# Performance work log

Measured on AMD Instinct MI355X. Metric: run time of the kernel, lower is better.

## Reference

```python
import jax, jax.numpy as jnp
import numpy as np

N = 20000      # nodes
C = 64         # in_channels
E = 640000     # edges (avg degree 32)
B = 8          # graphs in batch
STEPS = 16     # 2**4 diffusion steps per cascade
FENG = np.array([4, 8, 9, 12, 13, 14])  # feng_filters()


def make_wavelet():
    # Fixed 4x17 wavelet constructor: Psi_j = P^{2^{j-1}} - P^{2^j}
    W = jnp.zeros((4, 17), dtype=jnp.float32)
    W = W.at[0, 1].set(-1.0).at[0, 2].set(1.0)
    W = W.at[1, 2].set(-1.0).at[1, 4].set(1.0)
    W = W.at[2, 4].set(-1.0).at[2, 8].set(1.0)
    W = W.at[3, 8].set(-1.0).at[3, 16].set(1.0)
    return W


def setup_inputs() -> dict:
    key = jax.random.key(0)
    k1, k2, k3 = jax.random.split(key, 3)
    x = jax.random.normal(k1, (N, C), dtype=jnp.float32)
    edge_index = jax.random.randint(k2, (2, E), 0, N, dtype=jnp.int32)
    batch = jnp.sort(jax.random.randint(k3, (N,), 0, B, dtype=jnp.int32))
    wavelet_constructor = make_wavelet()
    return {"x": x, "edge_index": edge_index, "batch": batch,
            "wavelet_constructor": wavelet_constructor}


def _gcn_norm(edge_index, n, dtype):
    # Add self loops; norm = d^-1/2[row] * d^-1/2[col] (gcn_norm, weight 1)
    row, col = edge_index
    loop = jnp.arange(n, dtype=row.dtype)
    row = jnp.concatenate([row, loop])
    col = jnp.concatenate([col, loop])
    deg = jax.ops.segment_sum(jnp.ones_like(row, dtype=dtype), col, num_segments=n)
    dinv = jnp.where(deg > 0, jax.lax.rsqrt(deg), 0.0)
    return row, col, dinv[row] * dinv[col]


def _cascade(h0, row, col, norm, n):
    # 16 lazy-random-walk diffusion steps: h <- 0.5*(h + A_hat h); keep all levels.
    nb = norm.reshape((-1,) + (1,) * (h0.ndim - 1))
    def step(h, _):
        msg = jax.ops.segment_sum(h[row] * nb, col, num_segments=n)
        h = 0.5 * (h + msg)
        return h, h
    _, ys = jax.lax.scan(step, h0, None, length=STEPS)
    return jnp.concatenate([h0[None], ys], axis=0)  # [17, ...]


def reference(x, edge_index, batch, wavelet_constructor):
    n = x.shape[0]
    row, col, norm = _gcn_norm(edge_index, n, x.dtype)

    # First-order scattering
    S0 = x[:, :, None]                                       # [N, C, 1]
    lev1 = _cascade(S0, row, col, norm, n)                   # [17, N, C, 1]
    sub1 = jnp.einsum('wl,lnck->wnck', wavelet_constructor, lev1)[..., 0]  # [4, N, C]
    S1 = jnp.abs(jnp.transpose(sub1, (1, 2, 0)))             # [N, C, 4]

    # Second-order scattering
    lev2 = _cascade(S1, row, col, norm, n)                   # [17, N, C, 4]
    sub2 = jnp.einsum('wl,lncb->wncb', wavelet_constructor, lev2)          # [4, N, C, 4]
    S2_swapped = jnp.abs(jnp.transpose(sub2, (1, 0, 3, 2))).reshape(n, 16, -1)  # [N, 16, C]
    S2 = S2_swapped[:, FENG]                                 # [N, 6, C]

    feats = jnp.concatenate(
        [jnp.transpose(jnp.concatenate([S0, S1], axis=2), (0, 2, 1)), S2], axis=1)  # [N, 11, C]

    # Statistical-moments aggregation per graph
    d = feats.reshape(n, -1)                                 # [N, 11*C]
    cnt = jnp.maximum(jax.ops.segment_sum(jnp.ones((n,), d.dtype), batch,
                                          num_segments=B), 1.0)[:, None]
    mean = jax.ops.segment_sum(d, batch, num_segments=B) / cnt
    dev = d - mean[batch]
    var = jax.ops.segment_sum(dev ** 2, batch, num_segments=B) / cnt
    m3 = jax.ops.segment_sum(dev ** 3, batch, num_segments=B) / cnt
    m4 = jax.ops.segment_sum(dev ** 4, batch, num_segments=B) / cnt
    safe = var > 0
    vsafe = jnp.where(safe, var, 1.0)
    skew = jnp.where(safe, m3 / vsafe ** 1.5, 0.0)   # NaN (zero-var) -> 0
    kurt = jnp.where(safe, m4 / vsafe ** 2, -3.0)    # NaN (zero-var) -> -3
    out = jnp.concatenate([mean, var, skew, kurt], axis=1)   # [B, 4*11*C]
    return out, wavelet_constructor
```

## Files before the change

### kernel.cpp

```cpp
#include <hip/hip_runtime.h>
#include <hip/hip_fp16.h>

#define NB 8
#define CAP 128
#define NFEAT 704
#define MSLICE 8
#define PSLICE (MSLICE * 4)


__global__ void count_edges(const int* __restrict__ ei, int E, int* __restrict__ cnt) {
    int e = blockIdx.x * blockDim.x + threadIdx.x;
    if (e < E) atomicAdd(&cnt[ei[E + e]], 1);
}

__global__ void compute_dinv(const int* __restrict__ cnt, float* __restrict__ dinv, int n) {
    int v = blockIdx.x * blockDim.x + threadIdx.x;
    if (v < n) dinv[v] = rsqrtf((float)(cnt[v] + 1));
}

__global__ void fill_edges(const int* __restrict__ ei, int E, const float* __restrict__ dinv,
                           int* __restrict__ cursor, unsigned int* __restrict__ pairs) {
    int e = blockIdx.x * blockDim.x + threadIdx.x;
    if (e < E) {
        int r = ei[e], c = ei[E + e];
        int pos = atomicAdd(&cursor[c], 1);
        if (pos < CAP) {
            float w = dinv[r] * dinv[c];
            __half hw = __float2half_rn(w);
            unsigned short hb = *reinterpret_cast<unsigned short*>(&hw);
            pairs[(size_t)c * CAP + pos] = (unsigned int)(r & 0xFFFF) | ((unsigned int)hb << 16);
        }
    }
}

__global__ void pad_edges(const int* __restrict__ cnt, unsigned int* __restrict__ pairs, int n) {
    int v = blockIdx.x * blockDim.x + threadIdx.x;
    if (v >= n) return;
    int c = min(cnt[v], CAP);
    int c4 = (c + 3) & ~3;
    for (int j = c; j < c4; ++j) pairs[(size_t)v * CAP + j] = 0u;
}

__global__ void batch_bounds(const int* __restrict__ batch, int n, int* __restrict__ boff) {
    int i = blockIdx.x * blockDim.x + threadIdx.x;
    if (i >= n) return;
    int b = batch[i];
    int pb = (i == 0) ? -1 : batch[i - 1];
    for (int k = pb + 1; k <= b; ++k) boff[k] = i;
    if (i == n - 1) {
        for (int k = b + 1; k <= NB; ++k) boff[k] = n;
    }
}

__global__ void convert_f16(const float* __restrict__ x, unsigned short* __restrict__ xh, int n) {
    int i = blockIdx.x * blockDim.x + threadIdx.x;
    if (i < n) {
        __half h = __float2half_rn(x[i]);
        xh[i] = *reinterpret_cast<unsigned short*>(&h);
    }
}


__device__ __forceinline__ float h2f16(unsigned short h) {
    __half hh = *reinterpret_cast<__half*>(&h);
    return __half2float(hh);
}

__device__ __forceinline__ void fma_h4(float w, uint2 m, float* a) {
    float2 f0 = __half22float2(*reinterpret_cast<__half2*>(&m.x));
    float2 f1 = __half22float2(*reinterpret_cast<__half2*>(&m.y));
    a[0] += w * f0.x; a[1] += w * f0.y; a[2] += w * f1.x; a[3] += w * f1.y;
}

template <int NU>
__global__ __launch_bounds__(256) void cascade_k(
    const float* __restrict__ selfp, int sstride, long usz,
    const unsigned short* __restrict__ mirp, long musz,
    float* __restrict__ state_out, unsigned short* __restrict__ mir_out,
    const unsigned int* __restrict__ pairs, const int* __restrict__ cnt,
    const float* __restrict__ dinv, int n,
    int s,
    float* __restrict__ prevb,
    float* __restrict__ S1, unsigned short* __restrict__ S1h,
    float* __restrict__ S2)
{
    int lane = threadIdx.x & 63, widx = threadIdx.x >> 6;
    int node = blockIdx.x * 4 + widx;
    if (node >= n) return;
    node = __builtin_amdgcn_readfirstlane(node);

    int deg = min(cnt[node], CAP);
    int deg4 = (deg + 3) & ~3;
    float dv = dinv[node];
    float selfw = 1.f + dv * dv;

    int sub = lane >> 4;
    int cg  = lane & 15;

    const unsigned int* pb = pairs + (size_t)node * CAP;

    float a[NU][4];
#pragma unroll
    for (int u = 0; u < NU; ++u)
#pragma unroll
        for (int k = 0; k < 4; ++k) a[u][k] = 0.f;

    int j = 0;
    for (; j + 8 <= deg4; j += 8) {
        uint4 qA = *reinterpret_cast<const uint4*>(pb + j);
        uint4 qB = *reinterpret_cast<const uint4*>(pb + j + 4);
        unsigned int eA = sub < 2 ? (sub == 0 ? qA.x : qA.y) : (sub == 2 ? qA.z : qA.w);
        unsigned int eB = sub < 2 ? (sub == 0 ? qB.x : qB.y) : (sub == 2 ? qB.z : qB.w);
        int   sA = (int)(eA & 0xFFFFu);
        float wA = h2f16((unsigned short)(eA >> 16));
        int   sB = (int)(eB & 0xFFFFu);
        float wB = h2f16((unsigned short)(eB >> 16));
        uint2 gA[NU], gB[NU];
#pragma unroll
        for (int u = 0; u < NU; ++u)
            gA[u] = *reinterpret_cast<const uint2*>(mirp + (size_t)u * musz + (size_t)sA * 64 + cg * 4);
#pragma unroll
        for (int u = 0; u < NU; ++u)
            gB[u] = *reinterpret_cast<const uint2*>(mirp + (size_t)u * musz + (size_t)sB * 64 + cg * 4);
#pragma unroll
        for (int u = 0; u < NU; ++u) {
            fma_h4(wA, gA[u], a[u]);
            fma_h4(wB, gB[u], a[u]);
        }
    }
    if (j < deg4) {
        uint4 qA = *reinterpret_cast<const uint4*>(pb + j);
        unsigned int eA = sub < 2 ? (sub == 0 ? qA.x : qA.y) : (sub == 2 ? qA.z : qA.w);
        int   sA = (int)(eA & 0xFFFFu);
        float wA = h2f16((unsigned short)(eA >> 16));
        uint2 gA[NU];
#pragma unroll
        for (int u = 0; u < NU; ++u)
            gA[u] = *reinterpret_cast<const uint2*>(mirp + (size_t)u * musz + (size_t)sA * 64 + cg * 4);
#pragma unroll
        for (int u = 0; u < NU; ++u) fma_h4(wA, gA[u], a[u]);
    }

#pragma unroll
    for (int m = 16; m <= 32; m <<= 1) {
#pragma unroll
        for (int u = 0; u < NU; ++u) {
#pragma unroll
            for (int k = 0; k < 4; ++k) a[u][k] += __shfl_xor(a[u][k], m, 64);
        }
    }

    if (lane < 16) {
#pragma unroll
        for (int u = 0; u < NU; ++u) {
            const float* srow = selfp + (size_t)u * usz + (size_t)node * sstride + cg * 4;
            float4 hv = *reinterpret_cast<const float4*>(srow);
            float4 v;
            v.x = 0.5f * (selfw * hv.x + a[u][0]);
            v.y = 0.5f * (selfw * hv.y + a[u][1]);
            v.z = 0.5f * (selfw * hv.z + a[u][2]);
            v.w = 0.5f * (selfw * hv.w + a[u][3]);
            size_t oidx = (size_t)u * n * 64 + (size_t)node * 64 + cg * 4;
            *reinterpret_cast<float4*>(state_out + oidx) = v;
            __half2 p01 = __float22half2_rn(make_float2(v.x, v.y));
            __half2 p23 = __float22half2_rn(make_float2(v.z, v.w));
            uint2 mo;
            mo.x = *reinterpret_cast<unsigned int*>(&p01);
            mo.y = *reinterpret_cast<unsigned int*>(&p23);
            *reinterpret_cast<uint2*>(mir_out + oidx) = mo;

            int snap = (NU == 1) ? 1 : (2 << u);
            float* prow = prevb + oidx;
            if (s == snap) {
                *reinterpret_cast<float4*>(prow) = v;
            } else if (s > snap && (s == 2 || s == 4 || s == 8 || s == 16)) {
                float4 pv = *reinterpret_cast<const float4*>(prow);
                *reinterpret_cast<float4*>(prow) = v;
                float4 d;
                d.x = fabsf(v.x - pv.x); d.y = fabsf(v.y - pv.y);
                d.z = fabsf(v.z - pv.z); d.w = fabsf(v.w - pv.w);
                if (NU == 1) {
                    int slot = (s == 2) ? 0 : (s == 4) ? 1 : (s == 8) ? 2 : 3;
                    *reinterpret_cast<float4*>(S1 + (size_t)node * 256 + slot * 64 + cg * 4) = d;
                    if (slot < 3) {
                        __half2 d01 = __float22half2_rn(make_float2(d.x, d.y));
                        __half2 d23 = __float22half2_rn(make_float2(d.z, d.w));
                        uint2 dh;
                        dh.x = *reinterpret_cast<unsigned int*>(&d01);
                        dh.y = *reinterpret_cast<unsigned int*>(&d23);
                        *reinterpret_cast<uint2*>(S1h + (size_t)slot * n * 64 + (size_t)node * 64 + cg * 4) = dh;
                    }
                } else {
                    int slt;
                    if (u == 0)      slt = (s == 4) ? 0 : (s == 8) ? 1 : 3;
                    else if (u == 1) slt = (s == 8) ? 2 : 4;
                    else             slt = 5;
                    *reinterpret_cast<float4*>(S2 + (size_t)node * 384 + slt * 64 + cg * 4) = d;
                }
            }
        }
    }
}


__global__ __launch_bounds__(256) void moments_part(
    const float* __restrict__ x, const float* __restrict__ S1,
    const float* __restrict__ S2, const int* __restrict__ boff,
    double* __restrict__ part)
{
    int bid = blockIdx.x;
    int slice = bid % MSLICE;
    int k = (bid / MSLICE) % 11;
    int b = bid / (11 * MSLICE);
    int c = threadIdx.x & 63, sub = threadIdx.x >> 6;

    const float* base; int stride;
    if (k == 0)      { base = x  + c;                stride = 64;  }
    else if (k <= 4) { base = S1 + (k - 1) * 64 + c; stride = 256; }
    else             { base = S2 + (k - 5) * 64 + c; stride = 384; }

    int s0 = boff[b], s1e = boff[b + 1];
    int cntb = s1e - s0;
    int per = (cntb + MSLICE - 1) / MSLICE;
    int i0 = s0 + slice * per;
    int i1 = min(s1e, i0 + per);

    double a1 = 0, a2 = 0, a3 = 0, a4 = 0;
    for (int i = i0 + sub; i < i1; i += 4) {
        double v = (double)base[(size_t)i * stride];
        double qq = v * v;
        a1 += v; a2 += qq; a3 += qq * v; a4 += qq * qq;
    }
    int f = k * 64 + c;
    double* qp = part + ((((size_t)slice * 4 + sub) * NB + b) * NFEAT + f) * 4;
    qp[0] = a1; qp[1] = a2; qp[2] = a3; qp[3] = a4;
}

__global__ void finalize_k(const double* __restrict__ part, const int* __restrict__ boff,
                           const float* __restrict__ W, float* __restrict__ out) {
    int i = blockIdx.x * blockDim.x + threadIdx.x;
    if (i < NB * NFEAT) {
        int b = i / NFEAT, f = i % NFEAT;
        double s1 = 0, s2 = 0, s3 = 0, s4 = 0;
        for (int s = 0; s < PSLICE; ++s) {
            const double* qp = part + (((size_t)s * NB + b) * NFEAT + f) * 4;
            s1 += qp[0]; s2 += qp[1]; s3 += qp[2]; s4 += qp[3];
        }
        double cn = (double)max(boff[b + 1] - boff[b], 1);
        double mean = s1 / cn;
        double e2 = s2 / cn, e3 = s3 / cn, e4 = s4 / cn;
        double var = e2 - mean * mean;
        double m3 = e3 - 3.0 * mean * e2 + 2.0 * mean * mean * mean;
        double m4 = e4 - 4.0 * mean * e3 + 6.0 * mean * mean * e2 - 3.0 * mean * mean * mean * mean;
        float skew, kurt;
        if (var > 0.0) {
            double vs = var * sqrt(var);
            skew = (float)(m3 / vs);
            kurt = (float)(m4 / (var * var));
        } else {
            skew = 0.f; kurt = -3.f;
        }
        out[b * 2816 + f]        = (float)mean;
        out[b * 2816 + 704 + f]  = (float)var;
        out[b * 2816 + 1408 + f] = skew;
        out[b * 2816 + 2112 + f] = kurt;
    } else if (i < NB * NFEAT + 68) {
        int j = i - NB * NFEAT;
        out[NB * 2816 + j] = W[j];
    }
}


extern "C" void kernel_launch(void* const* d_in, const int* in_sizes, int n_in,
                              void* d_out, int out_size, void* d_ws, size_t ws_size,
                              hipStream_t stream) {
    const float* x     = (const float*)d_in[0];
    const int*   ei    = (const int*)d_in[1];
    const int*   batch = (const int*)d_in[2];
    const float* W     = (const float*)d_in[3];
    int N = in_sizes[0] / 64;
    int E = in_sizes[1] / 2;
    float* out = (float*)d_out;

    char* p = (char*)d_ws;
    auto alloc = [&](size_t bytes) { char* r = p; p += (bytes + 255) & ~255ULL; return r; };
    float* dinv  = (float*)alloc((size_t)N * 4);
    int*   cnt   = (int*)alloc((size_t)N * 4);
    int*   cursor= (int*)alloc((size_t)N * 4);
    int*   boff  = (int*)alloc((NB + 1) * 4);
    double* part = (double*)alloc((size_t)PSLICE * NB * NFEAT * 4 * 8);
    unsigned int* pairs = (unsigned int*)alloc((size_t)N * CAP * 4);
    float* S1    = (float*)alloc((size_t)N * 256 * 4);
    float* S2    = (float*)alloc((size_t)N * 384 * 4);
    unsigned short* S1h = (unsigned short*)alloc((size_t)3 * N * 64 * 2);
    unsigned short* xh  = (unsigned short*)alloc((size_t)N * 64 * 2);
    float* bufA  = (float*)alloc((size_t)3 * N * 64 * 4);
    float* bufB  = (float*)alloc((size_t)3 * N * 64 * 4);
    float* prev  = (float*)alloc((size_t)3 * N * 64 * 4);
    unsigned short* mirA = (unsigned short*)alloc((size_t)3 * N * 64 * 2);
    unsigned short* mirB = (unsigned short*)alloc((size_t)3 * N * 64 * 2);

    hipMemsetAsync(cnt, 0, (size_t)N * 4, stream);
    hipMemsetAsync(cursor, 0, (size_t)N * 4, stream);

    count_edges<<<(E + 255) / 256, 256, 0, stream>>>(ei, E, cnt);
    compute_dinv<<<(N + 255) / 256, 256, 0, stream>>>(cnt, dinv, N);
    fill_edges<<<(E + 255) / 256, 256, 0, stream>>>(ei, E, dinv, cursor, pairs);
    pad_edges<<<(N + 255) / 256, 256, 0, stream>>>(cnt, pairs, N);
    batch_bounds<<<(N + 255) / 256, 256, 0, stream>>>(batch, N, boff);
    convert_f16<<<(N * 64 + 255) / 256, 256, 0, stream>>>(x, xh, N * 64);

    long nu = (long)N * 64;
    int cgrid = (N + 3) / 4;

    for (int s = 1; s <= 16; ++s) {
        float* so = (s & 1) ? bufA : bufB;
        unsigned short* mo = (s & 1) ? mirA : mirB;
        const float* selfp; int sstride; long usz;
        const unsigned short* mirp; long musz;
        if (s == 1) { selfp = x; sstride = 64; usz = 0; mirp = xh; musz = 0; }
        else {
            selfp = (s & 1) ? bufB : bufA; sstride = 64; usz = nu;
            mirp = (s & 1) ? mirB : mirA; musz = nu;
        }
        cascade_k<1><<<cgrid, 256, 0, stream>>>(selfp, sstride, usz, mirp, musz, so, mo,
                                                pairs, cnt, dinv, N, s, prev, S1, S1h, S2);
    }

    for (int s = 1; s <= 16; ++s) {
        float* so = (s & 1) ? bufA : bufB;
        unsigned short* mo = (s & 1) ? mirA : mirB;
        const float* selfp; int sstride; long usz;
        const unsigned short* mirp; long musz;
        if (s == 1) { selfp = S1; sstride = 256; usz = 64; mirp = S1h; musz = nu; }
        else {
            selfp = (s & 1) ? bufB : bufA; sstride = 64; usz = nu;
            mirp = (s & 1) ? mirB : mirA; musz = nu;
        }
        cascade_k<3><<<cgrid, 256, 0, stream>>>(selfp, sstride, usz, mirp, musz, so, mo,
                                                pairs, cnt, dinv, N, s, prev, S1, S1h, S2);
    }

    moments_part<<<NB * 11 * MSLICE, 256, 0, stream>>>(x, S1, S2, boff, part);

    int fin_threads = NB * NFEAT + 68;
    finalize_k<<<(fin_threads + 255) / 256, 256, 0, stream>>>(part, boff, W, out);
}
```

Before: 939.9 us.

## Split 3-wide second-order cascade into per-channel single passes with prefetched edge loop

```diff
diff --git a/kernel.cpp b/kernel.cpp
--- a/kernel.cpp
+++ b/kernel.cpp
@@ -37,8 +37,8 @@
     int v = blockIdx.x * blockDim.x + threadIdx.x;
     if (v >= n) return;
     int c = min(cnt[v], CAP);
-    int c4 = (c + 3) & ~3;
-    for (int j = c; j < c4; ++j) pairs[(size_t)v * CAP + j] = 0u;
+    int c8 = (c + 7) & ~7;
+    for (int j = c; j < c8; ++j) pairs[(size_t)v * CAP + j] = 0u;
 }
 
 __global__ void batch_bounds(const int* __restrict__ batch, int n, int* __restrict__ boff) {
@@ -72,17 +72,25 @@
     a[0] += w * f0.x; a[1] += w * f0.y; a[2] += w * f1.x; a[3] += w * f1.y;
 }
 
-template <int NU>
-__global__ __launch_bounds__(256) void cascade_k(
-    const float* __restrict__ selfp, int sstride, long usz,
-    const unsigned short* __restrict__ mirp, long musz,
-    float* __restrict__ state_out, unsigned short* __restrict__ mir_out,
+__device__ __forceinline__ uint2 pack_h4(float4 v) {
+    __half2 p01 = __float22half2_rn(make_float2(v.x, v.y));
+    __half2 p23 = __float22half2_rn(make_float2(v.z, v.w));
+    uint2 r;
+    r.x = *reinterpret_cast<unsigned int*>(&p01);
+    r.y = *reinterpret_cast<unsigned int*>(&p23);
+    return r;
+}
+
+__global__ __launch_bounds__(256) void cascade1(
+    const float* __restrict__ selfp, int sstride,
+    const unsigned short* __restrict__ mirp,
+    float* __restrict__ stateo, unsigned short* __restrict__ miro,
+    float* __restrict__ prevb,
     const unsigned int* __restrict__ pairs, const int* __restrict__ cnt,
     const float* __restrict__ dinv, int n,
-    int s,
-    float* __restrict__ prevb,
-    float* __restrict__ S1, unsigned short* __restrict__ S1h,
-    float* __restrict__ S2)
+    int mode, int slot,
+    float* __restrict__ Sdst, int sostride,
+    unsigned short* __restrict__ Shdst)
 {
     int lane = threadIdx.x & 63, widx = threadIdx.x >> 6;
     int node = blockIdx.x * 4 + widx;
@@ -90,7 +98,7 @@
     node = __builtin_amdgcn_readfirstlane(node);
 
     int deg = min(cnt[node], CAP);
-    int deg4 = (deg + 3) & ~3;
+    int deg8 = (deg + 7) & ~7;
     float dv = dinv[node];
     float selfw = 1.f + dv * dv;
 
@@ -99,105 +107,63 @@
 
     const unsigned int* pb = pairs + (size_t)node * CAP;
 
-    float a[NU][4];
-#pragma unroll
-    for (int u = 0; u < NU; ++u)
-#pragma unroll
-        for (int k = 0; k < 4; ++k) a[u][k] = 0.f;
-
-    int j = 0;
-    for (; j + 8 <= deg4; j += 8) {
-        uint4 qA = *reinterpret_cast<const uint4*>(pb + j);
-        uint4 qB = *reinterpret_cast<const uint4*>(pb + j + 4);
-        unsigned int eA = sub < 2 ? (sub == 0 ? qA.x : qA.y) : (sub == 2 ? qA.z : qA.w);
-        unsigned int eB = sub < 2 ? (sub == 0 ? qB.x : qB.y) : (sub == 2 ? qB.z : qB.w);
-        int   sA = (int)(eA & 0xFFFFu);
-        float wA = h2f16((unsigned short)(eA >> 16));
-        int   sB = (int)(eB & 0xFFFFu);
-        float wB = h2f16((unsigned short)(eB >> 16));
-        uint2 gA[NU], gB[NU];
-#pragma unroll
-        for (int u = 0; u < NU; ++u)
-            gA[u] = *reinterpret_cast<const uint2*>(mirp + (size_t)u * musz + (size_t)sA * 64 + cg * 4);
-#pragma unroll
-        for (int u = 0; u < NU; ++u)
-            gB[u] = *reinterpret_cast<const uint2*>(mirp + (size_t)u * musz + (size_t)sB * 64 + cg * 4);
-#pragma unroll
-        for (int u = 0; u < NU; ++u) {
-            fma_h4(wA, gA[u], a[u]);
-            fma_h4(wB, gB[u], a[u]);
-        }
-    }
-    if (j < deg4) {
-        uint4 qA = *reinterpret_cast<const uint4*>(pb + j);
-        unsigned int eA = sub < 2 ? (sub == 0 ? qA.x : qA.y) : (sub == 2 ? qA.z : qA.w);
-        int   sA = (int)(eA & 0xFFFFu);
-        float wA = h2f16((unsigned short)(eA >> 16));
-        uint2 gA[NU];
-#pragma unroll
-        for (int u = 0; u < NU; ++u)
-            gA[u] = *reinterpret_cast<const uint2*>(mirp + (size_t)u * musz + (size_t)sA * 64 + cg * 4);
-#pragma unroll
-        for (int u = 0; u < NU; ++u) fma_h4(wA, gA[u], a[u]);
+    float a[4] = {0.f, 0.f, 0.f, 0.f};
+
+    if (deg8 > 0) {
+        uint4 qA = *reinterpret_cast<const uint4*>(pb);
+        uint4 qB = *reinterpret_cast<const uint4*>(pb + 4);
+        int j = 0;
+        while (true) {
+            int jn = j + 8;
+            bool more = jn < deg8;
+            uint4 nA, nB;
+            if (more) {
+                nA = *reinterpret_cast<const uint4*>(pb + jn);
+                nB = *reinterpret_cast<const uint4*>(pb + jn + 4);
+            }
+            unsigned int eA = sub < 2 ? (sub == 0 ? qA.x : qA.y) : (sub == 2 ? qA.z : qA.w);
+            unsigned int eB = sub < 2 ? (sub == 0 ? qB.x : qB.y) : (sub == 2 ? qB.z : qB.w);
+            int   sA = (int)(eA & 0xFFFFu);
+            float wA = h2f16((unsigned short)(eA >> 16));
+            int   sB = (int)(eB & 0xFFFFu);
+            float wB = h2f16((unsigned short)(eB >> 16));
+            uint2 gA = *reinterpret_cast<const uint2*>(mirp + (size_t)sA * 64 + cg * 4);
+            uint2 gB = *reinterpret_cast<const uint2*>(mirp + (size_t)sB * 64 + cg * 4);
+            fma_h4(wA, gA, a);
+            fma_h4(wB, gB, a);
+            if (!more) break;
+            qA = nA; qB = nB; j = jn;
+        }
     }
 
 #pragma unroll
     for (int m = 16; m <= 32; m <<= 1) {
 #pragma unroll
-        for (int u = 0; u < NU; ++u) {
-#pragma unroll
-            for (int k = 0; k < 4; ++k) a[u][k] += __shfl_xor(a[u][k], m, 64);
-        }
+        for (int k = 0; k < 4; ++k) a[k] += __shfl_xor(a[k], m, 64);
     }
 
     if (lane < 16) {
-#pragma unroll
-        for (int u = 0; u < NU; ++u) {
-            const float* srow = selfp + (size_t)u * usz + (size_t)node * sstride + cg * 4;
-            float4 hv = *reinterpret_cast<const float4*>(srow);
-            float4 v;
-            v.x = 0.5f * (selfw * hv.x + a[u][0]);
-            v.y = 0.5f * (selfw * hv.y + a[u][1]);
-            v.z = 0.5f * (selfw * hv.z + a[u][2]);
-            v.w = 0.5f * (selfw * hv.w + a[u][3]);
-            size_t oidx = (size_t)u * n * 64 + (size_t)node * 64 + cg * 4;
-            *reinterpret_cast<float4*>(state_out + oidx) = v;
-            __half2 p01 = __float22half2_rn(make_float2(v.x, v.y));
-            __half2 p23 = __float22half2_rn(make_float2(v.z, v.w));
-            uint2 mo;
-            mo.x = *reinterpret_cast<unsigned int*>(&p01);
-            mo.y = *reinterpret_cast<unsigned int*>(&p23);
-            *reinterpret_cast<uint2*>(mir_out + oidx) = mo;
-
-            int snap = (NU == 1) ? 1 : (2 << u);
-            float* prow = prevb + oidx;
-            if (s == snap) {
-                *reinterpret_cast<float4*>(prow) = v;
-            } else if (s > snap && (s == 2 || s == 4 || s == 8 || s == 16)) {
-                float4 pv = *reinterpret_cast<const float4*>(prow);
-                *reinterpret_cast<float4*>(prow) = v;
-                float4 d;
-                d.x = fabsf(v.x - pv.x); d.y = fabsf(v.y - pv.y);
-                d.z = fabsf(v.z - pv.z); d.w = fabsf(v.w - pv.w);
-                if (NU == 1) {
-                    int slot = (s == 2) ? 0 : (s == 4) ? 1 : (s == 8) ? 2 : 3;
-                    *reinterpret_cast<float4*>(S1 + (size_t)node * 256 + slot * 64 + cg * 4) = d;
-                    if (slot < 3) {
-                        __half2 d01 = __float22half2_rn(make_float2(d.x, d.y));
-                        __half2 d23 = __float22half2_rn(make_float2(d.z, d.w));
-                        uint2 dh;
-                        dh.x = *reinterpret_cast<unsigned int*>(&d01);
-                        dh.y = *reinterpret_cast<unsigned int*>(&d23);
-                        *reinterpret_cast<uint2*>(S1h + (size_t)slot * n * 64 + (size_t)node * 64 + cg * 4) = dh;
-                    }
-                } else {
-                    int slt;
-                    if (u == 0)      slt = (s == 4) ? 0 : (s == 8) ? 1 : 3;
-                    else if (u == 1) slt = (s == 8) ? 2 : 4;
-                    else             slt = 5;
-                    *reinterpret_cast<float4*>(S2 + (size_t)node * 384 + slt * 64 + cg * 4) = d;
-                }
-            }
+        float4 hv = *reinterpret_cast<const float4*>(selfp + (size_t)node * sstride + cg * 4);
+        float4 v;
+        v.x = 0.5f * (selfw * hv.x + a[0]);
+        v.y = 0.5f * (selfw * hv.y + a[1]);
+        v.z = 0.5f * (selfw * hv.z + a[2]);
+        v.w = 0.5f * (selfw * hv.w + a[3]);
+        size_t oidx = (size_t)node * 64 + cg * 4;
+        *reinterpret_cast<float4*>(stateo + oidx) = v;
+        *reinterpret_cast<uint2*>(miro + oidx) = pack_h4(v);
+        float* prow = prevb + oidx;
+        if (mode == 1) {
+            *reinterpret_cast<float4*>(prow) = v;
+        } else if (mode == 2) {
+            float4 pv = *reinterpret_cast<const float4*>(prow);
+            *reinterpret_cast<float4*>(prow) = v;
+            float4 d;
+            d.x = fabsf(v.x - pv.x); d.y = fabsf(v.y - pv.y);
+            d.z = fabsf(v.z - pv.z); d.w = fabsf(v.w - pv.w);
+            *reinterpret_cast<float4*>(Sdst + (size_t)node * sostride + slot * 64 + cg * 4) = d;
+            if (Shdst)
+                *reinterpret_cast<uint2*>(Shdst + oidx) = pack_h4(d);
         }
     }
 }
@@ -292,13 +258,14 @@
     unsigned int* pairs = (unsigned int*)alloc((size_t)N * CAP * 4);
     float* S1    = (float*)alloc((size_t)N * 256 * 4);
     float* S2    = (float*)alloc((size_t)N * 384 * 4);
-    unsigned short* S1h = (unsigned short*)alloc((size_t)3 * N * 64 * 2);
-    unsigned short* xh  = (unsigned short*)alloc((size_t)N * 64 * 2);
-    float* bufA  = (float*)alloc((size_t)3 * N * 64 * 4);
-    float* bufB  = (float*)alloc((size_t)3 * N * 64 * 4);
-    float* prev  = (float*)alloc((size_t)3 * N * 64 * 4);
-    unsigned short* mirA = (unsigned short*)alloc((size_t)3 * N * 64 * 2);
-    unsigned short* mirB = (unsigned short*)alloc((size_t)3 * N * 64 * 2);
+    long nu = (long)N * 64;
+    unsigned short* s1h = (unsigned short*)alloc((size_t)3 * nu * 2);
+    unsigned short* xh  = (unsigned short*)alloc((size_t)nu * 2);
+    float* bA    = (float*)alloc((size_t)nu * 4);
+    float* bB    = (float*)alloc((size_t)nu * 4);
+    unsigned short* hA = (unsigned short*)alloc((size_t)nu * 2);
+    unsigned short* hB = (unsigned short*)alloc((size_t)nu * 2);
+    float* prev  = (float*)alloc((size_t)nu * 4);
 
     hipMemsetAsync(cnt, 0, (size_t)N * 4, stream);
     hipMemsetAsync(cursor, 0, (size_t)N * 4, stream);
@@ -308,37 +275,46 @@
     fill_edges<<<(E + 255) / 256, 256, 0, stream>>>(ei, E, dinv, cursor, pairs);
     pad_edges<<<(N + 255) / 256, 256, 0, stream>>>(cnt, pairs, N);
     batch_bounds<<<(N + 255) / 256, 256, 0, stream>>>(batch, N, boff);
-    convert_f16<<<(N * 64 + 255) / 256, 256, 0, stream>>>(x, xh, N * 64);
-
-    long nu = (long)N * 64;
+    convert_f16<<<((int)nu + 255) / 256, 256, 0, stream>>>(x, xh, (int)nu);
+
     int cgrid = (N + 3) / 4;
 
     for (int s = 1; s <= 16; ++s) {
-        float* so = (s & 1) ? bufA : bufB;
-        unsigned short* mo = (s & 1) ? mirA : mirB;
-        const float* selfp; int sstride; long usz;
-        const unsigned short* mirp; long musz;
-        if (s == 1) { selfp = x; sstride = 64; usz = 0; mirp = xh; musz = 0; }
-        else {
-            selfp = (s & 1) ? bufB : bufA; sstride = 64; usz = nu;
-            mirp = (s & 1) ? mirB : mirA; musz = nu;
-        }
-        cascade_k<1><<<cgrid, 256, 0, stream>>>(selfp, sstride, usz, mirp, musz, so, mo,
-                                                pairs, cnt, dinv, N, s, prev, S1, S1h, S2);
-    }
-
-    for (int s = 1; s <= 16; ++s) {
-        float* so = (s & 1) ? bufA : bufB;
-        unsigned short* mo = (s & 1) ? mirA : mirB;
-        const float* selfp; int sstride; long usz;
-        const unsigned short* mirp; long musz;
-        if (s == 1) { selfp = S1; sstride = 256; usz = 64; mirp = S1h; musz = nu; }
-        else {
-            selfp = (s & 1) ? bufB : bufA; sstride = 64; usz = nu;
-            mirp = (s & 1) ? mirB : mirA; musz = nu;
-        }
-        cascade_k<3><<<cgrid, 256, 0, stream>>>(selfp, sstride, usz, mirp, musz, so, mo,
-                                                pairs, cnt, dinv, N, s, prev, S1, S1h, S2);
+        const float* si = (s == 1) ? x  : ((s & 1) ? bB : bA);
+        const unsigned short* mi = (s == 1) ? xh : ((s & 1) ? hB : hA);
+        float* so = (s & 1) ? bA : bB;
+        unsigned short* mo = (s & 1) ? hA : hB;
+        int mode = 0, slot = 0;
+        if (s == 1) mode = 1;
+        else if (s == 2 || s == 4 || s == 8 || s == 16) {
+            mode = 2;
+            slot = (s == 2) ? 0 : (s == 4) ? 1 : (s == 8) ? 2 : 3;
+        }
+        unsigned short* shd = (mode == 2 && slot < 3) ? (s1h + (size_t)slot * nu) : nullptr;
+        cascade1<<<cgrid, 256, 0, stream>>>(si, (s == 1) ? 64 : 64, mi, so, mo, prev,
+                                            pairs, cnt, dinv, N, mode, slot, S1, 256, shd);
+    }
+
+    for (int u = 0; u < 3; ++u) {
+        int snap = 2 << u;
+        for (int f = 1; f <= 16; ++f) {
+            const float* si; int sstride;
+            const unsigned short* mi;
+            if (f == 1) { si = S1 + u * 64; sstride = 256; mi = s1h + (size_t)u * nu; }
+            else        { si = (f & 1) ? bB : bA; sstride = 64; mi = (f & 1) ? hB : hA; }
+            float* so = (f & 1) ? bA : bB;
+            unsigned short* mo = (f & 1) ? hA : hB;
+            int mode = 0, slot = 0;
+            if (f == snap) mode = 1;
+            else if (f > snap && (f == 4 || f == 8 || f == 16)) {
+                mode = 2;
+                if (u == 0)      slot = (f == 4) ? 0 : (f == 8) ? 1 : 3;
+                else if (u == 1) slot = (f == 8) ? 2 : 4;
+                else             slot = 5;
+            }
+            cascade1<<<cgrid, 256, 0, stream>>>(si, sstride, mi, so, mo, prev,
+                                                pairs, cnt, dinv, N, mode, slot, S2, 384, nullptr);
+        }
     }
 
     moments_part<<<NB * 11 * MSLICE, 256, 0, stream>>>(x, S1, S2, boff, part);
```

New measurement: 1.153 ms. +22.7%, slower.
